# Optimization experiments

Measured on AMD Instinct MI355X. Metric: run time of the kernel, lower is better.

Reference implementation:

```python
import jax, jax.numpy as jnp
import numpy as np

HEADS = 16
DIM_HEAD = 64
SCALE = DIM_HEAD ** -0.5


def setup_inputs() -> dict:
    key = jax.random.key(0)
    k1, k2, k3, k4 = jax.random.split(key, 4)
    b, n, dim = 2, 2048, 1024
    inner = HEADS * DIM_HEAD  # 1024
    return {
        "x": jax.random.normal(k1, (b, n, dim), dtype=jnp.float32),
        "x1": jax.random.normal(k2, (b, n, dim), dtype=jnp.float32),
        "W_qkv": jax.random.normal(k3, (dim, inner * 3), dtype=jnp.float32) * (dim ** -0.5),
        "W_out": jax.random.normal(k4, (inner, dim), dtype=jnp.float32) * (inner ** -0.5),
        "b_out": jnp.zeros((dim,), dtype=jnp.float32),
    }


def _split_heads(t):
    b, n, hd = t.shape
    return t.reshape(b, n, HEADS, DIM_HEAD).transpose(0, 2, 1, 3)  # b h n d


def _merge_heads(t):
    b, h, n, d = t.shape
    return t.transpose(0, 2, 1, 3).reshape(b, n, h * d)


def reference(x, x1, W_qkv, W_out, b_out):
    qkv = jnp.split(x @ W_qkv, 3, axis=-1)
    qkv1 = jnp.split(x1 @ W_qkv, 3, axis=-1)
    q, k, v = map(_split_heads, qkv)
    q1, k1, v1 = map(_split_heads, qkv1)

    # cross attention: x queries attend to x1 keys/values, and vice versa
    attn = jax.nn.softmax(jnp.einsum('bhnd,bhmd->bhnm', q, k1) * SCALE, axis=-1)
    attn1 = jax.nn.softmax(jnp.einsum('bhnd,bhmd->bhnm', q1, k) * SCALE, axis=-1)
    out = _merge_heads(jnp.einsum('bhnm,bhmd->bhnd', attn, v1))
    out1 = _merge_heads(jnp.einsum('bhnm,bhmd->bhnd', attn1, v))

    out = out @ W_out + b_out
    out1 = out1 @ W_out + b_out
    return out, out1
```

## Files before the change

kernel.cpp:

```cpp
#include <hip/hip_runtime.h>
#include <hip/hip_bf16.h>


typedef __attribute__((ext_vector_type(8))) short short8;
typedef __attribute__((ext_vector_type(4))) float f32x4;

#define MFMA_BF16(a, b, c) __builtin_amdgcn_mfma_f32_16x16x32_bf16((a), (b), (c), 0, 0, 0)

__device__ __forceinline__ ushort f2bf(float f) {
    __hip_bfloat16 h = __float2bfloat16(f);
    return *reinterpret_cast<ushort*>(&h);
}

__device__ __forceinline__ void gload_lds16(const void* g, void* l) {
    __builtin_amdgcn_global_load_lds(
        (const __attribute__((address_space(1))) void*)g,
        (__attribute__((address_space(3))) void*)l, 16, 0, 0);
}

__global__ __launch_bounds__(256) void cvt2_k(const float* __restrict__ a,
                                              const float* __restrict__ b,
                                              ushort* __restrict__ out) {
    const int idx = blockIdx.x * 256 + threadIdx.x;
    const int half = 1048576;
    const float* src = (idx < half) ? a : b;
    const int i = (idx < half ? idx : idx - half) * 4;
    float4 v = *(const float4*)(src + i);
    ushort4 o;
    o.x = f2bf(v.x); o.y = f2bf(v.y); o.z = f2bf(v.z); o.w = f2bf(v.w);
    *(ushort4*)(out + (size_t)idx * 4) = o;
}

__global__ __launch_bounds__(256) void transpose_cvt(const float* __restrict__ in,
                                                     ushort* __restrict__ out,
                                                     int R, int C) {
    __shared__ ushort tile[32][33];
    const int c0 = blockIdx.x * 32, r0 = blockIdx.y * 32;
    const int tx = threadIdx.x, ty = threadIdx.y;
#pragma unroll
    for (int i = 0; i < 4; ++i)
        tile[ty * 4 + i][tx] = f2bf(in[(size_t)(r0 + ty * 4 + i) * C + c0 + tx]);
    __syncthreads();
#pragma unroll
    for (int i = 0; i < 4; ++i)
        out[(size_t)(c0 + ty * 4 + i) * R + r0 + tx] = tile[tx][ty * 4 + i];
}

__global__ __launch_bounds__(256) void qkv_gemm(const ushort* __restrict__ xb,
                                                const ushort* __restrict__ wt,
                                                ushort* __restrict__ qb,
                                                ushort* __restrict__ kb,
                                                ushort* __restrict__ vb) {
    __shared__ __align__(16) ushort As[128 * 64];
    __shared__ __align__(16) ushort Bs[128 * 64];

    const int n0 = blockIdx.x * 128;
    const int m0 = blockIdx.y * 128;
    const int t = threadIdx.x;
    const int lane = t & 63, w = t >> 6;
    const int wm = (w >> 1) * 64, wn = (w & 1) * 64;
    const int l16 = lane & 15, lq = lane >> 4;

    const int srow = lane >> 3;
    const int scol = ((lane & 7) * 16) ^ (srow << 4);

    f32x4 acc[4][4] = {};

    for (int k0 = 0; k0 < 1024; k0 += 64) {
        __syncthreads();
#pragma unroll
        for (int c = 0; c < 4; ++c) {
            const int ch = w * 4 + c;
            const int row = ch * 8 + srow;
            gload_lds16((const char*)xb + ((size_t)(m0 + row) * 1024 + k0) * 2 + scol,
                        (char*)As + ch * 1024);
            gload_lds16((const char*)wt + ((size_t)(n0 + row) * 1024 + k0) * 2 + scol,
                        (char*)Bs + ch * 1024);
        }
        __syncthreads();
#pragma unroll
        for (int kc = 0; kc < 2; ++kc) {
            short8 a[4], b[4];
#pragma unroll
            for (int i = 0; i < 4; ++i) {
                const int row = wm + i * 16 + l16;
                a[i] = *(const short8*)((const char*)As + row * 128 +
                                        ((kc * 64 + lq * 16) ^ ((row & 7) << 4)));
            }
#pragma unroll
            for (int j = 0; j < 4; ++j) {
                const int row = wn + j * 16 + l16;
                b[j] = *(const short8*)((const char*)Bs + row * 128 +
                                        ((kc * 64 + lq * 16) ^ ((row & 7) << 4)));
            }
#pragma unroll
            for (int i = 0; i < 4; ++i)
#pragma unroll
                for (int j = 0; j < 4; ++j) acc[i][j] = MFMA_BF16(a[i], b[j], acc[i][j]);
        }
    }

    const int which = (n0 >> 10);
    const float qscale = (which == 0) ? 0.125f : 1.0f;

#pragma unroll
    for (int i = 0; i < 4; ++i) {
#pragma unroll
        for (int jj = 0; jj < 4; ++jj) {
#pragma unroll
            for (int rr = 0; rr < 4; ++rr) {
                const int m = m0 + wm + i * 16 + lq * 4 + rr;
                const int nc = n0 + wn + jj * 16 + l16;
                const ushort bv = f2bf(acc[i][jj][rr] * qscale);
                const int s = m >> 12;
                const int mm = m & 4095;
                const int rem = nc & 1023;
                const int h = rem >> 6, d = rem & 63;
                const int sb = (s << 1) | (mm >> 11);
                const int pos = mm & 2047;
                const size_t bh = (size_t)(sb * 16 + h);
                if (which == 0)      qb[(bh * 2048 + pos) * 64 + d] = bv;
                else if (which == 1) kb[(bh * 2048 + pos) * 64 + d] = bv;
                else                 vb[(bh * 64 + d) * 2048 + pos] = bv;
            }
        }
    }
}

__global__ __launch_bounds__(256, 4) void attn_k(const ushort* __restrict__ qb,
                                                 const ushort* __restrict__ kb,
                                                 const ushort* __restrict__ vb,
                                                 ushort* __restrict__ ob) {
    __shared__ __align__(16) ushort Ks[2][4096];
    __shared__ __align__(16) ushort Vs[2][4096];
    __shared__ __align__(16) ushort Pt[4][1024];

    const int t = threadIdx.x, lane = t & 63, w = t >> 6;
    const int l16 = lane & 15, lq = lane >> 4;

    const int lid = blockIdx.x;
    const int xcd = lid & 7, kk = lid >> 3;
    const int qt = kk & 15;
    const int g = xcd + ((kk >> 4) << 3);
    const int h = g & 15, sb = g >> 4;
    const int s = sb >> 1, bb = sb & 1;
    const int kvsb = ((1 - s) << 1) | bb;
    const int q0 = qt * 128 + w * 32;

    const ushort* qp = qb + (size_t)(sb * 16 + h) * 2048 * 64;
    const char* kp = (const char*)(kb + (size_t)(kvsb * 16 + h) * 2048 * 64);
    const char* vp = (const char*)(vb + (size_t)(kvsb * 16 + h) * 64 * 2048);

    short8 aq[2][2];
#pragma unroll
    for (int u = 0; u < 2; ++u)
#pragma unroll
        for (int c = 0; c < 2; ++c)
            aq[u][c] = *(const short8*)(qp + (size_t)(q0 + u * 16 + l16) * 64 + c * 32 + lq * 8);

    short8 ones;
#pragma unroll
    for (int j = 0; j < 8; ++j) ones[j] = (short)0x3F80;

    f32x4 o_acc[2][4] = {};
    f32x4 l_acc[2] = {};

    const int swl = ((lane >> 3) & 7) << 4;
    auto stage = [&](int buf, int key0) {
#pragma unroll
        for (int i = 0; i < 2; ++i) {
            const int ch = w * 2 + i;
            const int off = ch * 1024 + lane * 16;
            gload_lds16(kp + (size_t)key0 * 128 + (off ^ swl),
                        (char*)&Ks[buf][0] + ch * 1024);
            const int rd = ch * 8 + (lane >> 3);
            const int cb = (lane & 7) * 16;
            gload_lds16(vp + (size_t)rd * 4096 + (size_t)key0 * 2 + (cb ^ swl),
                        (char*)&Vs[buf][0] + ch * 1024);
        }
    };

    stage(0, 0);
    __syncthreads();

    char* Pw = (char*)&Pt[w][0];

    for (int tt = 0; tt < 32; ++tt) {
        const int cur = tt & 1;
        if (tt < 31) stage(cur ^ 1, (tt + 1) * 64);

        const char* Kc = (const char*)&Ks[cur][0];
        const char* Vc = (const char*)&Vs[cur][0];

        f32x4 sc0[4] = {}, sc1[4] = {};
#pragma unroll
        for (int j = 0; j < 4; ++j) {
            const int row = j * 16 + l16;
            const int swr = (row & 7) << 4;
            short8 k0 = *(const short8*)(Kc + row * 128 + ((lq * 16) ^ swr));
            short8 k1 = *(const short8*)(Kc + row * 128 + ((64 + lq * 16) ^ swr));
            sc0[j] = MFMA_BF16(aq[0][0], k0, sc0[j]);
            sc0[j] = MFMA_BF16(aq[0][1], k1, sc0[j]);
            sc1[j] = MFMA_BF16(aq[1][0], k0, sc1[j]);
            sc1[j] = MFMA_BF16(aq[1][1], k1, sc1[j]);
        }

        short8 ap[2][2];
#pragma unroll
        for (int j = 0; j < 4; ++j)
#pragma unroll
            for (int r2 = 0; r2 < 4; ++r2) {
                const int row = lq * 4 + r2;
                *(ushort*)(Pw + row * 128 + ((j * 32 + l16 * 2) ^ ((row & 7) << 4))) =
                    f2bf(__expf(sc0[j][r2]));
            }
        asm volatile("s_waitcnt lgkmcnt(0)" ::: "memory");
        {
            const int swr = (l16 & 7) << 4;
            ap[0][0] = *(const short8*)(Pw + l16 * 128 + ((lq * 16) ^ swr));
            ap[0][1] = *(const short8*)(Pw + l16 * 128 + ((64 + lq * 16) ^ swr));
        }
        asm volatile("s_waitcnt lgkmcnt(0)" ::: "memory");
#pragma unroll
        for (int j = 0; j < 4; ++j)
#pragma unroll
            for (int r2 = 0; r2 < 4; ++r2) {
                const int row = lq * 4 + r2;
                *(ushort*)(Pw + row * 128 + ((j * 32 + l16 * 2) ^ ((row & 7) << 4))) =
                    f2bf(__expf(sc1[j][r2]));
            }
        asm volatile("s_waitcnt lgkmcnt(0)" ::: "memory");
        {
            const int swr = (l16 & 7) << 4;
            ap[1][0] = *(const short8*)(Pw + l16 * 128 + ((lq * 16) ^ swr));
            ap[1][1] = *(const short8*)(Pw + l16 * 128 + ((64 + lq * 16) ^ swr));
        }

        l_acc[0] = MFMA_BF16(ap[0][0], ones, l_acc[0]);
        l_acc[0] = MFMA_BF16(ap[0][1], ones, l_acc[0]);
        l_acc[1] = MFMA_BF16(ap[1][0], ones, l_acc[1]);
        l_acc[1] = MFMA_BF16(ap[1][1], ones, l_acc[1]);
#pragma unroll
        for (int dt = 0; dt < 4; ++dt) {
            const int row = dt * 16 + l16;
            const int swr = (row & 7) << 4;
            short8 v0 = *(const short8*)(Vc + row * 128 + ((lq * 16) ^ swr));
            short8 v1 = *(const short8*)(Vc + row * 128 + ((64 + lq * 16) ^ swr));
            o_acc[0][dt] = MFMA_BF16(ap[0][0], v0, o_acc[0][dt]);
            o_acc[0][dt] = MFMA_BF16(ap[0][1], v1, o_acc[0][dt]);
            o_acc[1][dt] = MFMA_BF16(ap[1][0], v0, o_acc[1][dt]);
            o_acc[1][dt] = MFMA_BF16(ap[1][1], v1, o_acc[1][dt]);
        }

        __syncthreads();
    }

#pragma unroll
    for (int u = 0; u < 2; ++u) {
        float inv[4];
#pragma unroll
        for (int r2 = 0; r2 < 4; ++r2) inv[r2] = 1.f / l_acc[u][r2];
#pragma unroll
        for (int dt = 0; dt < 4; ++dt)
#pragma unroll
            for (int r2 = 0; r2 < 4; ++r2)
                ob[(size_t)(sb * 2048 + q0 + u * 16 + lq * 4 + r2) * 1024 + h * 64 + dt * 16 + l16] =
                    f2bf(o_acc[u][dt][r2] * inv[r2]);
    }
}

__global__ __launch_bounds__(256) void out_gemm(const ushort* __restrict__ ob,
                                                const ushort* __restrict__ wot,
                                                const float* __restrict__ bias,
                                                float* __restrict__ out) {
    __shared__ __align__(16) ushort As[128 * 64];
    __shared__ __align__(16) ushort Bs[128 * 64];

    const int n0 = blockIdx.x * 128;
    const int m0 = blockIdx.y * 128;
    const int t = threadIdx.x;
    const int lane = t & 63, w = t >> 6;
    const int wm = (w >> 1) * 64, wn = (w & 1) * 64;
    const int l16 = lane & 15, lq = lane >> 4;

    const int srow = lane >> 3;
    const int scol = ((lane & 7) * 16) ^ (srow << 4);

    f32x4 acc[4][4] = {};

    for (int k0 = 0; k0 < 1024; k0 += 64) {
        __syncthreads();
#pragma unroll
        for (int c = 0; c < 4; ++c) {
            const int ch = w * 4 + c;
            const int row = ch * 8 + srow;
            gload_lds16((const char*)ob + ((size_t)(m0 + row) * 1024 + k0) * 2 + scol,
                        (char*)As + ch * 1024);
            gload_lds16((const char*)wot + ((size_t)(n0 + row) * 1024 + k0) * 2 + scol,
                        (char*)Bs + ch * 1024);
        }
        __syncthreads();
#pragma unroll
        for (int kc = 0; kc < 2; ++kc) {
            short8 a[4], b[4];
#pragma unroll
            for (int i = 0; i < 4; ++i) {
                const int row = wm + i * 16 + l16;
                a[i] = *(const short8*)((const char*)As + row * 128 +
                                        ((kc * 64 + lq * 16) ^ ((row & 7) << 4)));
            }
#pragma unroll
            for (int j = 0; j < 4; ++j) {
                const int row = wn + j * 16 + l16;
                b[j] = *(const short8*)((const char*)Bs + row * 128 +
                                        ((kc * 64 + lq * 16) ^ ((row & 7) << 4)));
            }
#pragma unroll
            for (int i = 0; i < 4; ++i)
#pragma unroll
                for (int j = 0; j < 4; ++j) acc[i][j] = MFMA_BF16(a[i], b[j], acc[i][j]);
        }
    }

    float biasf[4];
#pragma unroll
    for (int jj = 0; jj < 4; ++jj) biasf[jj] = bias[n0 + wn + jj * 16 + l16];

#pragma unroll
    for (int i = 0; i < 4; ++i)
#pragma unroll
        for (int jj = 0; jj < 4; ++jj)
#pragma unroll
            for (int rr = 0; rr < 4; ++rr) {
                const int m = m0 + wm + i * 16 + lq * 4 + rr;
                const int nc = n0 + wn + jj * 16 + l16;
                out[(size_t)m * 1024 + nc] = acc[i][jj][rr] + biasf[jj];
            }
}

extern "C" void kernel_launch(void* const* d_in, const int* in_sizes, int n_in,
                              void* d_out, int out_size, void* d_ws, size_t ws_size,
                              hipStream_t stream) {
    (void)out_size; (void)ws_size;
    const float *x = nullptr, *x1 = nullptr, *wqkv = nullptr, *wout = nullptr, *bias = nullptr;
    for (int i = 0; i < n_in; ++i) {
        const int sz = in_sizes[i];
        const float* p = (const float*)d_in[i];
        if (sz == 4194304)      { if (!x) x = p; else x1 = p; }
        else if (sz == 3145728) wqkv = p;
        else if (sz == 1048576) wout = p;
        else if (sz == 1024)    bias = p;
    }
    float* out = (float*)d_out;

    ushort* ws      = (ushort*)d_ws;
    ushort* wqkv_t  = ws;
    ushort* wout_t  = wqkv_t + 3072 * 1024;
    ushort* xb      = wout_t + 1024 * 1024;
    ushort* qbuf    = xb + 8388608;
    ushort* kbuf    = qbuf + 8388608;
    ushort* vbuf    = kbuf + 8388608;
    ushort* obuf    = xb;

    cvt2_k<<<8192, 256, 0, stream>>>(x, x1, xb);
    transpose_cvt<<<dim3(96, 32), dim3(32, 8), 0, stream>>>(wqkv, wqkv_t, 1024, 3072);
    transpose_cvt<<<dim3(32, 32), dim3(32, 8), 0, stream>>>(wout, wout_t, 1024, 1024);
    qkv_gemm<<<dim3(24, 64), 256, 0, stream>>>(xb, wqkv_t, qbuf, kbuf, vbuf);
    attn_k<<<1024, 256, 0, stream>>>(qbuf, kbuf, vbuf, obuf);
    out_gemm<<<dim3(8, 64), 256, 0, stream>>>(obuf, wout_t, bias, out);
}
```

Baseline: 306.6 us.

## Compute transposed S with 32x32 MFMA and feed P via lane shuffles

The attention kernel now computes S^T = K·Q^T with 32x32x16 bf16 MFMA, so each lane holds the scores for one query column. It packs exp(S) into bf16 registers and swaps halves across lanes with shuffles to build the PV operand directly. This removes the per-wave LDS round trip for P, its waitcnt barriers, and the ones-matrix MFMA for row sums, which become plain register adds. The two weight transpose launches are also merged into one kernel to save a launch. Register pressure rises with the larger accumulators, which may affect occupancy at 4 waves per SIMD.

```diff
diff --git a/kernel.cpp b/kernel.cpp
--- a/kernel.cpp
+++ b/kernel.cpp
@@ -4,12 +4,18 @@
 
 typedef __attribute__((ext_vector_type(8))) short short8;
 typedef __attribute__((ext_vector_type(4))) float f32x4;
+typedef __attribute__((ext_vector_type(16))) float f32x16;
 
 #define MFMA_BF16(a, b, c) __builtin_amdgcn_mfma_f32_16x16x32_bf16((a), (b), (c), 0, 0, 0)
+#define MFMA32(a, b, c)    __builtin_amdgcn_mfma_f32_32x32x16_bf16((a), (b), (c), 0, 0, 0)
 
 __device__ __forceinline__ ushort f2bf(float f) {
     __hip_bfloat16 h = __float2bfloat16(f);
     return *reinterpret_cast<ushort*>(&h);
+}
+
+__device__ __forceinline__ unsigned pk2(float a, float b) {
+    return (unsigned)f2bf(a) | ((unsigned)f2bf(b) << 16);
 }
 
 __device__ __forceinline__ void gload_lds16(const void* g, void* l) {
@@ -31,11 +37,17 @@
     *(ushort4*)(out + (size_t)idx * 4) = o;
 }
 
-__global__ __launch_bounds__(256) void transpose_cvt(const float* __restrict__ in,
-                                                     ushort* __restrict__ out,
-                                                     int R, int C) {
+__global__ __launch_bounds__(256) void transpose_cvt2(const float* __restrict__ wqkv,
+                                                      ushort* __restrict__ wqkv_t,
+                                                      const float* __restrict__ wout,
+                                                      ushort* __restrict__ wout_t) {
     __shared__ ushort tile[32][33];
-    const int c0 = blockIdx.x * 32, r0 = blockIdx.y * 32;
+    int bx = blockIdx.x;
+    const float* in; ushort* out; int C;
+    if (bx < 96) { in = wqkv; out = wqkv_t; C = 3072; }
+    else         { bx -= 96; in = wout; out = wout_t; C = 1024; }
+    const int R = 1024;
+    const int c0 = bx * 32, r0 = blockIdx.y * 32;
     const int tx = threadIdx.x, ty = threadIdx.y;
 #pragma unroll
     for (int i = 0; i < 4; ++i)
@@ -133,10 +145,9 @@
                                                  ushort* __restrict__ ob) {
     __shared__ __align__(16) ushort Ks[2][4096];
     __shared__ __align__(16) ushort Vs[2][4096];
-    __shared__ __align__(16) ushort Pt[4][1024];
 
     const int t = threadIdx.x, lane = t & 63, w = t >> 6;
-    const int l16 = lane & 15, lq = lane >> 4;
+    const int l31 = lane & 31, hi = lane >> 5;
 
     const int lid = blockIdx.x;
     const int xcd = lid & 7, kk = lid >> 3;
@@ -151,19 +162,13 @@
     const char* kp = (const char*)(kb + (size_t)(kvsb * 16 + h) * 2048 * 64);
     const char* vp = (const char*)(vb + (size_t)(kvsb * 16 + h) * 64 * 2048);
 
-    short8 aq[2][2];
-#pragma unroll
-    for (int u = 0; u < 2; ++u)
-#pragma unroll
-        for (int c = 0; c < 2; ++c)
-            aq[u][c] = *(const short8*)(qp + (size_t)(q0 + u * 16 + l16) * 64 + c * 32 + lq * 8);
-
-    short8 ones;
-#pragma unroll
-    for (int j = 0; j < 8; ++j) ones[j] = (short)0x3F80;
-
-    f32x4 o_acc[2][4] = {};
-    f32x4 l_acc[2] = {};
+    short8 qf[4];
+#pragma unroll
+    for (int c = 0; c < 4; ++c)
+        qf[c] = *(const short8*)(qp + (size_t)(q0 + l31) * 64 + c * 16 + hi * 8);
+
+    f32x16 o0 = {}, o1 = {};
+    float lsum = 0.f;
 
     const int swl = ((lane >> 3) & 7) << 4;
     auto stage = [&](int buf, int key0) {
@@ -183,89 +188,76 @@
     stage(0, 0);
     __syncthreads();
 
-    char* Pw = (char*)&Pt[w][0];
-
     for (int tt = 0; tt < 32; ++tt) {
         const int cur = tt & 1;
         if (tt < 31) stage(cur ^ 1, (tt + 1) * 64);
 
         const char* Kc = (const char*)&Ks[cur][0];
         const char* Vc = (const char*)&Vs[cur][0];
-
-        f32x4 sc0[4] = {}, sc1[4] = {};
-#pragma unroll
-        for (int j = 0; j < 4; ++j) {
-            const int row = j * 16 + l16;
-            const int swr = (row & 7) << 4;
-            short8 k0 = *(const short8*)(Kc + row * 128 + ((lq * 16) ^ swr));
-            short8 k1 = *(const short8*)(Kc + row * 128 + ((64 + lq * 16) ^ swr));
-            sc0[j] = MFMA_BF16(aq[0][0], k0, sc0[j]);
-            sc0[j] = MFMA_BF16(aq[0][1], k1, sc0[j]);
-            sc1[j] = MFMA_BF16(aq[1][0], k0, sc1[j]);
-            sc1[j] = MFMA_BF16(aq[1][1], k1, sc1[j]);
-        }
-
-        short8 ap[2][2];
-#pragma unroll
-        for (int j = 0; j < 4; ++j)
-#pragma unroll
-            for (int r2 = 0; r2 < 4; ++r2) {
-                const int row = lq * 4 + r2;
-                *(ushort*)(Pw + row * 128 + ((j * 32 + l16 * 2) ^ ((row & 7) << 4))) =
-                    f2bf(__expf(sc0[j][r2]));
-            }
-        asm volatile("s_waitcnt lgkmcnt(0)" ::: "memory");
+        const int sw = (l31 & 7) << 4;
+
+        f32x16 scA = {}, scB = {};
+#pragma unroll
+        for (int c = 0; c < 4; ++c) {
+            const int off = c * 32 + hi * 16;
+            short8 ka = *(const short8*)(Kc + l31 * 128 + (off ^ sw));
+            short8 kb2 = *(const short8*)(Kc + (32 + l31) * 128 + (off ^ sw));
+            scA = MFMA32(ka, qf[c], scA);
+            scB = MFMA32(kb2, qf[c], scB);
+        }
+
+#pragma unroll
+        for (int r = 0; r < 16; ++r) scA[r] = __expf(scA[r]);
+#pragma unroll
+        for (int r = 0; r < 16; ++r) scB[r] = __expf(scB[r]);
         {
-            const int swr = (l16 & 7) << 4;
-            ap[0][0] = *(const short8*)(Pw + l16 * 128 + ((lq * 16) ^ swr));
-            ap[0][1] = *(const short8*)(Pw + l16 * 128 + ((64 + lq * 16) ^ swr));
-        }
-        asm volatile("s_waitcnt lgkmcnt(0)" ::: "memory");
-#pragma unroll
-        for (int j = 0; j < 4; ++j)
-#pragma unroll
-            for (int r2 = 0; r2 < 4; ++r2) {
-                const int row = lq * 4 + r2;
-                *(ushort*)(Pw + row * 128 + ((j * 32 + l16 * 2) ^ ((row & 7) << 4))) =
-                    f2bf(__expf(sc1[j][r2]));
-            }
-        asm volatile("s_waitcnt lgkmcnt(0)" ::: "memory");
-        {
-            const int swr = (l16 & 7) << 4;
-            ap[1][0] = *(const short8*)(Pw + l16 * 128 + ((lq * 16) ^ swr));
-            ap[1][1] = *(const short8*)(Pw + l16 * 128 + ((64 + lq * 16) ^ swr));
-        }
-
-        l_acc[0] = MFMA_BF16(ap[0][0], ones, l_acc[0]);
-        l_acc[0] = MFMA_BF16(ap[0][1], ones, l_acc[0]);
-        l_acc[1] = MFMA_BF16(ap[1][0], ones, l_acc[1]);
-        l_acc[1] = MFMA_BF16(ap[1][1], ones, l_acc[1]);
-#pragma unroll
-        for (int dt = 0; dt < 4; ++dt) {
-            const int row = dt * 16 + l16;
-            const int swr = (row & 7) << 4;
-            short8 v0 = *(const short8*)(Vc + row * 128 + ((lq * 16) ^ swr));
-            short8 v1 = *(const short8*)(Vc + row * 128 + ((64 + lq * 16) ^ swr));
-            o_acc[0][dt] = MFMA_BF16(ap[0][0], v0, o_acc[0][dt]);
-            o_acc[0][dt] = MFMA_BF16(ap[0][1], v1, o_acc[0][dt]);
-            o_acc[1][dt] = MFMA_BF16(ap[1][0], v0, o_acc[1][dt]);
-            o_acc[1][dt] = MFMA_BF16(ap[1][1], v1, o_acc[1][dt]);
-        }
-
-        __syncthreads();
-    }
-
-#pragma unroll
-    for (int u = 0; u < 2; ++u) {
-        float inv[4];
-#pragma unroll
-        for (int r2 = 0; r2 < 4; ++r2) inv[r2] = 1.f / l_acc[u][r2];
-#pragma unroll
-        for (int dt = 0; dt < 4; ++dt)
-#pragma unroll
-            for (int r2 = 0; r2 < 4; ++r2)
-                ob[(size_t)(sb * 2048 + q0 + u * 16 + lq * 4 + r2) * 1024 + h * 64 + dt * 16 + l16] =
-                    f2bf(o_acc[u][dt][r2] * inv[r2]);
+            float sA = (((scA[0] + scA[1]) + (scA[2] + scA[3])) +
+                        ((scA[4] + scA[5]) + (scA[6] + scA[7]))) +
+                       (((scA[8] + scA[9]) + (scA[10] + scA[11])) +
+                        ((scA[12] + scA[13]) + (scA[14] + scA[15])));
+            float sB = (((scB[0] + scB[1]) + (scB[2] + scB[3])) +
+                        ((scB[4] + scB[5]) + (scB[6] + scB[7]))) +
+                       (((scB[8] + scB[9]) + (scB[10] + scB[11])) +
+                        ((scB[12] + scB[13]) + (scB[14] + scB[15])));
+            lsum += sA + sB;
+        }
+
+#define PACK_PV(P, BASE, KS)                                                     \
+        {                                                                        \
+            unsigned R00 = pk2(P[BASE + 0], P[BASE + 1]);                        \
+            unsigned R10 = pk2(P[BASE + 2], P[BASE + 3]);                        \
+            unsigned R01 = pk2(P[BASE + 4], P[BASE + 5]);                        \
+            unsigned R11 = pk2(P[BASE + 6], P[BASE + 7]);                        \
+            unsigned ra = (unsigned)__shfl_xor((int)(hi ? R00 : R01), 32);       \
+            unsigned rb = (unsigned)__shfl_xor((int)(hi ? R10 : R11), 32);       \
+            union { unsigned u[4]; short8 s8; } ap;                              \
+            ap.u[0] = hi ? ra : R00;                                             \
+            ap.u[1] = hi ? rb : R10;                                             \
+            ap.u[2] = hi ? R01 : ra;                                             \
+            ap.u[3] = hi ? R11 : rb;                                             \
+            const int vo = (KS) * 32 + hi * 16;                                  \
+            short8 v0 = *(const short8*)(Vc + l31 * 128 + (vo ^ sw));            \
+            short8 v1 = *(const short8*)(Vc + (32 + l31) * 128 + (vo ^ sw));     \
+            o0 = MFMA32(ap.s8, v0, o0);                                          \
+            o1 = MFMA32(ap.s8, v1, o1);                                          \
+        }
+        PACK_PV(scA, 0, 0)
+        PACK_PV(scA, 8, 1)
+        PACK_PV(scB, 0, 2)
+        PACK_PV(scB, 8, 3)
+#undef PACK_PV
+
+        __syncthreads();
+    }
+
+    const float lf = lsum + __shfl_xor(lsum, 32);
+    const size_t obase = (size_t)(sb * 2048 + q0) * 1024 + h * 64 + l31;
+#pragma unroll
+    for (int r = 0; r < 16; ++r) {
+        const int qrow = (r & 3) + 8 * (r >> 2) + 4 * hi;
+        const float invl = 1.f / __shfl(lf, qrow);
+        ob[obase + (size_t)qrow * 1024]      = f2bf(o0[r] * invl);
+        ob[obase + (size_t)qrow * 1024 + 32] = f2bf(o1[r] * invl);
     }
 }
 
@@ -363,8 +355,7 @@
     ushort* obuf    = xb;
 
     cvt2_k<<<8192, 256, 0, stream>>>(x, x1, xb);
-    transpose_cvt<<<dim3(96, 32), dim3(32, 8), 0, stream>>>(wqkv, wqkv_t, 1024, 3072);
-    transpose_cvt<<<dim3(32, 32), dim3(32, 8), 0, stream>>>(wout, wout_t, 1024, 1024);
+    transpose_cvt2<<<dim3(128, 32), dim3(32, 8), 0, stream>>>(wqkv, wqkv_t, wout, wout_t);
     qkv_gemm<<<dim3(24, 64), 256, 0, stream>>>(xb, wqkv_t, qbuf, kbuf, vbuf);
     attn_k<<<1024, 256, 0, stream>>>(qbuf, kbuf, vbuf, obuf);
     out_gemm<<<dim3(8, 64), 256, 0, stream>>>(obuf, wout_t, bias, out);
```

Measured after the change: 307.3 us. Within noise of the previous version (+0.3%).
